# Kernel tuning notes

Measured on AMD Instinct MI355X. Metric: run time of the kernel, lower is better.

Reference implementation:

```python
import jax, jax.numpy as jnp
import numpy as np

B, L, D_IN, H, N, NL = 16, 5000, 12, 256, 32, 4  # N = d_state//2 complex modes


def layer_norm(x, g, b, eps=1e-5):
    m = x.mean(-1, keepdims=True)
    v = ((x - m) ** 2).mean(-1, keepdims=True)
    return (x - m) * jax.lax.rsqrt(v + eps) * g + b


def s4d_kernel(log_dt, logA_re, A_im, Cp, length):
    # S4D-style diagonal SSM kernel (ZOH discretization), conjugate-symmetric -> 2*real
    dt = jnp.exp(log_dt)                      # (H,)
    A = -jnp.exp(logA_re) + 1j * A_im         # (H, N)
    C = Cp[..., 0] + 1j * Cp[..., 1]          # (H, N)
    dtA = A * dt[:, None]                     # (H, N)
    Ct = C * (jnp.exp(dtA) - 1.0) / A         # (H, N)
    V = jnp.exp(dtA[:, :, None] * jnp.arange(length, dtype=log_dt.dtype))  # (H, N, L) Vandermonde
    return 2.0 * jnp.einsum('hn,hnl->hl', Ct, V).real  # (H, L)


def s4_block(u, log_dt, logA_re, A_im, Cp, D, W_glu, b_glu):
    # u: (B, L, H), transposed=False convention
    length = u.shape[1]
    K = s4d_kernel(log_dt, logA_re, A_im, Cp, length)     # (H, L)
    n_fft = 2 * length
    k_f = jnp.fft.rfft(K, n=n_fft)                        # (H, F)
    u_f = jnp.fft.rfft(u, n=n_fft, axis=1)                # (B, F, H)
    y = jnp.fft.irfft(u_f * k_f.T[None], n=n_fft, axis=1)[:, :length]  # causal conv
    y = y + u * D                                         # skip connection
    y = jax.nn.gelu(y)
    y = y @ W_glu + b_glu                                 # (B, L, 2H)
    return jax.nn.glu(y, axis=-1)                         # (B, L, H)


def setup_inputs() -> dict:
    key = jax.random.key(0)
    ks = jax.random.split(key, 8)
    dt_min, dt_max = 1e-3, 1e-1
    log_dt = np.log(dt_min) + jax.random.uniform(ks[2], (NL, H)) * (np.log(dt_max) - np.log(dt_min))
    A_im = jnp.broadcast_to(np.pi * jnp.arange(N, dtype=jnp.float32), (NL, H, N)).copy()
    return {
        'x': jax.random.normal(ks[0], (B, L, D_IN), jnp.float32),
        'W_in': jax.random.normal(ks[1], (D_IN, H), jnp.float32) / np.sqrt(D_IN),
        'b_in': jnp.zeros((H,), jnp.float32),
        'ln_g': jnp.ones((NL, H), jnp.float32),
        'ln_b': jnp.zeros((NL, H), jnp.float32),
        'log_dt': log_dt.astype(jnp.float32),
        'logA_re': jnp.full((NL, H, N), np.log(0.5), jnp.float32),
        'A_im': A_im,
        'Cp': jax.random.normal(ks[3], (NL, H, N, 2), jnp.float32) * (0.5 ** 0.5),
        'D': jax.random.normal(ks[4], (NL, H), jnp.float32),
        'W_glu': jax.random.normal(ks[5], (NL, H, 2 * H), jnp.float32) / np.sqrt(H),
        'b_glu': jnp.zeros((NL, 2 * H), jnp.float32),
        'fn_g': jnp.ones((H,), jnp.float32),
        'fn_b': jnp.zeros((H,), jnp.float32),
    }


def reference(x, W_in, b_in, ln_g, ln_b, log_dt, logA_re, A_im, Cp, D, W_glu, b_glu, fn_g, fn_b):
    x = x @ W_in + b_in  # (B, L, H)
    for i in range(NL):
        z = layer_norm(x, ln_g[i], ln_b[i])  # prenorm
        residual = z
        y = s4_block(z, log_dt[i], logA_re[i], A_im[i], Cp[i], D[i], W_glu[i], b_glu[i])
        x = y + residual  # dropout is identity in eval
    return layer_norm(x, fn_g, fn_b)
```

## Files before the change

### kernel.cpp

```cpp
#include <hip/hip_runtime.h>
#include <math.h>

#define BB 16
#define LL 5000
#define DIN 12
#define HH 256
#define NN 32
#define NLAYER 4
#define LC 128
#define NCH 40
#define TAIL 8
#define COLS (BB*NCH)
#define NROWS (BB*LL)
#define KU 192

typedef __attribute__((ext_vector_type(8))) _Float16 f16x8;
typedef __attribute__((ext_vector_type(4))) float f32x4;

__device__ __forceinline__ float fast_gelu(float a) {
  float z = fmaf(0.0713548163f * a, a * a, 1.5957691216f * a);
  float e = __expf(-z);
  return a * __builtin_amdgcn_rcpf(1.0f + e);
}

__device__ __forceinline__ unsigned pk2h(float a, float b) {
  union { _Float16 h[2]; unsigned u; } x;
  x.h[0] = (_Float16)a; x.h[1] = (_Float16)b;
  return x.u;
}

__device__ __forceinline__ float2 upk2(unsigned u) {
  union { unsigned u; _Float16 h[2]; } x;
  x.u = u;
  return make_float2((float)x.h[0], (float)x.h[1]);
}

__global__ __launch_bounds__(128) void paramT_kernel(
    const float* __restrict__ log_dt, const float* __restrict__ logA_re,
    const float* __restrict__ A_im, const float* __restrict__ Cp,
    const float* __restrict__ Dv, int l,
    _Float16* __restrict__ Tc, _Float16* __restrict__ V, float* __restrict__ WLc) {
  int h = blockIdx.x;
  int t = threadIdx.x;
  __shared__ float s_are[NN], s_aim[NN], s_cre[NN], s_cim[NN];
  __shared__ float s_K[128];
  if (t < NN) {
    int n = t;
    int idx = (l * HH + h) * NN + n;
    float dt = expf(log_dt[l * HH + h]);
    float Are = -expf(logA_re[idx]);
    float Aim = A_im[idx];
    float are = Are * dt, aim = Aim * dt;
    float e = expf(are);
    float wre = e * cosf(aim), wim = e * sinf(aim);
    float cr = Cp[2 * idx], ci = Cp[2 * idx + 1];
    float nre = wre - 1.0f, nim = wim;
    float tre = cr * nre - ci * nim;
    float tim = cr * nim + ci * nre;
    float inv = 1.0f / (Are * Are + Aim * Aim);
    s_are[n] = are; s_aim[n] = aim;
    s_cre[n] = 2.0f * (tre * Are + tim * Aim) * inv;
    s_cim[n] = 2.0f * (tim * Are - tre * Aim) * inv;
    float eL = expf(128.0f * are);
    float ang = 128.0f * aim;
    WLc[h * 64 + 2 * n] = eL * cosf(ang);
    WLc[h * 64 + 2 * n + 1] = eL * sinf(ang);
  }
  __syncthreads();
  {
    float ksum = 0.0f;
    unsigned* brow = (unsigned*)(Tc + ((size_t)h * 128 + t) * KU + 128);
    for (int n = 0; n < NN; n++) {
      float are = s_are[n], aim = s_aim[n];
      float cre = s_cre[n], cim = s_cim[n];
      float ft = (float)t;
      float E = expf(are * ft);
      float a = aim * ft;
      float wtre = E * cosf(a), wtim = E * sinf(a);
      ksum = fmaf(cre, wtre, ksum);
      ksum = fmaf(-cim, wtim, ksum);
      float ew = expf(are);
      float wre = ew * cosf(aim), wim = ew * sinf(aim);
      float wpre = wtre * wre - wtim * wim;
      float wpim = wtre * wim + wtim * wre;
      float bre = cre * wpre - cim * wpim;
      float bim = -(cre * wpim + cim * wpre);
      brow[n] = pk2h(bre, bim);
      float fk = (float)(127 - t);
      float E2 = expf(are * fk);
      float a2 = aim * fk;
      V[((size_t)h * 64 + 2 * n) * 128 + t] = (_Float16)(E2 * cosf(a2));
      V[((size_t)h * 64 + 2 * n + 1) * 128 + t] = (_Float16)(E2 * sinf(a2));
    }
    s_K[t] = ksum;
  }
  __syncthreads();
  float D = Dv[l * HH + h];
  unsigned* row = (unsigned*)(Tc + ((size_t)h * 128 + t) * KU);
  for (int q = 0; q < 64; q++) {
    float v0 = 0.0f, v1 = 0.0f;
    int d0 = t - 2 * q;
    int d1 = d0 - 1;
    if (d0 >= 0) v0 = s_K[d0] + (d0 == 0 ? D : 0.0f);
    if (d1 >= 0) v1 = s_K[d1] + (d1 == 0 ? D : 0.0f);
    row[q] = pk2h(v0, v1);
  }
}

__global__ __launch_bounds__(256) void wt_kernel(
    const float* __restrict__ W, _Float16* __restrict__ Wt) {
  int gid = blockIdx.x * 256 + threadIdx.x;
  int l = gid >> 9, col = gid & 511;
  const float* w = W + (size_t)l * HH * 512 + col;
  _Float16* o = Wt + (size_t)gid * HH;
  for (int k = 0; k < HH; k++) o[k] = (_Float16)(w[(size_t)k * 512]);
}

__global__ __launch_bounds__(256) void proj_kernel(
    const float* __restrict__ x, const float* __restrict__ Win,
    const float* __restrict__ bin, _Float16* __restrict__ X) {
  int tp = threadIdx.x & 127, rs = threadIdx.x >> 7;
  int h0 = 2 * tp;
  float w0[DIN], w1[DIN];
#pragma unroll
  for (int k = 0; k < DIN; k++) {
    w0[k] = Win[k * HH + h0];
    w1[k] = Win[k * HH + h0 + 1];
  }
  float b0 = bin[h0], b1 = bin[h0 + 1];
  for (int row = blockIdx.x * 2 + rs; row < NROWS; row += gridDim.x * 2) {
    float a0 = b0, a1 = b1;
#pragma unroll
    for (int k = 0; k < DIN; k++) {
      float xv = x[(size_t)row * DIN + k];
      a0 = fmaf(xv, w0[k], a0);
      a1 = fmaf(xv, w1[k], a1);
    }
    *(unsigned*)(X + (size_t)row * HH + h0) = pk2h(a0, a1);
  }
}

__global__ __launch_bounds__(256) void ln_kernel(
    const _Float16* __restrict__ in, float* __restrict__ out,
    const float* __restrict__ g, const float* __restrict__ b) {
  int wave = threadIdx.x >> 6, lane = threadIdx.x & 63;
  int row = blockIdx.x * 4 + wave;
  uint2 pv = *(const uint2*)(in + (size_t)row * HH + 4 * lane);
  float2 v01 = upk2(pv.x), v23 = upk2(pv.y);
  float s = v01.x + v01.y + v23.x + v23.y;
  float q = v01.x * v01.x + v01.y * v01.y + v23.x * v23.x + v23.y * v23.y;
#pragma unroll
  for (int m = 1; m < 64; m <<= 1) { s += __shfl_xor(s, m); q += __shfl_xor(q, m); }
  float mean = s * (1.0f / HH);
  float var = q * (1.0f / HH) - mean * mean;
  float rstd = rsqrtf(var + 1e-5f);
  float4 gg = ((const float4*)g)[lane];
  float4 bb = ((const float4*)b)[lane];
  float4 o;
  o.x = (v01.x - mean) * rstd * gg.x + bb.x;
  o.y = (v01.y - mean) * rstd * gg.y + bb.y;
  o.z = (v23.x - mean) * rstd * gg.z + bb.z;
  o.w = (v23.y - mean) * rstd * gg.w + bb.w;
  ((float4*)(out + (size_t)row * HH))[lane] = o;
}

__global__ __launch_bounds__(256) void lnU_kernel(
    _Float16* __restrict__ stream, _Float16* __restrict__ U,
    const float* __restrict__ g, const float* __restrict__ b) {
  __shared__ unsigned short Ut[64][260];
  int col = blockIdx.x;
  int bI = col / NCH, cI = col % NCH;
  int len = (cI == NCH - 1) ? TAIL : 128;
  int wave = threadIdx.x >> 6, lane = threadIdx.x & 63;
  float4 gg = ((const float4*)g)[lane];
  float4 bv = ((const float4*)b)[lane];
  size_t base = ((size_t)bI * LL + (size_t)cI * 128) * HH;
#pragma unroll
  for (int half = 0; half < 2; half++) {
    if (half) __syncthreads();
    int t0 = half * 64;
    int lenh = len - t0;
    lenh = lenh < 0 ? 0 : (lenh > 64 ? 64 : lenh);
    for (int idx = threadIdx.x; idx < (64 - lenh) * 260; idx += 256) {
      int r = idx / 260;
      Ut[lenh + r][idx - r * 260] = 0;
    }
    for (int it = 0; it < 16; it++) {
      int tl = it * 4 + wave;
      if (tl < lenh) {
        int tau = t0 + tl;
        uint2 pv = *(const uint2*)(stream + base + (size_t)tau * HH + 4 * lane);
        float2 v01 = upk2(pv.x), v23 = upk2(pv.y);
        float s = v01.x + v01.y + v23.x + v23.y;
        float q = v01.x * v01.x + v01.y * v01.y + v23.x * v23.x + v23.y * v23.y;
#pragma unroll
        for (int m = 1; m < 64; m <<= 1) { s += __shfl_xor(s, m); q += __shfl_xor(q, m); }
        float mean = s * (1.0f / HH);
        float var = q * (1.0f / HH) - mean * mean;
        float rstd = rsqrtf(var + 1e-5f);
        float o0 = (v01.x - mean) * rstd * gg.x + bv.x;
        float o1 = (v01.y - mean) * rstd * gg.y + bv.y;
        float o2 = (v23.x - mean) * rstd * gg.z + bv.z;
        float o3 = (v23.y - mean) * rstd * gg.w + bv.w;
        uint2 p;
        p.x = pk2h(o0, o1);
        p.y = pk2h(o2, o3);
        *(uint2*)(stream + base + (size_t)tau * HH + 4 * lane) = p;
        *(uint2*)&Ut[tl][4 * lane] = p;
      }
    }
    __syncthreads();
    for (int rep = 0; rep < 8; rep++) {
      int linear = rep * 256 + threadIdx.x;
      int h = linear >> 3, ub = linear & 7;
      unsigned* dst = (unsigned*)(U + ((size_t)h * COLS + col) * KU) + half * 32;
#pragma unroll
      for (int s2 = 0; s2 < 4; s2++) {
        int u = ub + s2 * 8;
        dst[u] = (unsigned)Ut[2 * u][h] | ((unsigned)Ut[2 * u + 1][h] << 16);
      }
    }
  }
}

__global__ __launch_bounds__(256) void gemmAC_kernel(
    const _Float16* __restrict__ V, _Float16* __restrict__ U,
    const float* __restrict__ WLc) {
  __shared__ float smf[4096];
  _Float16* As = (_Float16*)smf;
  _Float16* Bs = As + 64 * 72;
  float* Ps = smf;
  int h = blockIdx.x, b = blockIdx.y;
  int t = threadIdx.x;
  int w = t >> 6, lane = t & 63, lr = lane & 15, quad = lane >> 4;
  f32x4 acc[3];
#pragma unroll
  for (int j = 0; j < 3; j++) acc[j] = (f32x4)(0.0f);

  for (int kt = 0; kt < 128; kt += 64) {
#pragma unroll
    for (int i = 0; i < 2; i++) {
      int idx = t + 256 * i;
      int m = idx >> 3, q = idx & 7;
      *(uint4*)&As[m * 72 + q * 8] =
          *(const uint4*)(V + ((size_t)h * 64 + m) * 128 + kt + q * 8);
    }
#pragma unroll
    for (int i = 0; i < 2; i++) {
      int idx = t + 256 * i;
      if (idx < 384) {
        int jj = idx >> 3, q = idx & 7;
        uint4 v = make_uint4(0u, 0u, 0u, 0u);
        if (jj < NCH)
          v = *(const uint4*)(U + ((size_t)h * COLS + (size_t)b * NCH + jj) * KU + kt + q * 8);
        *(uint4*)&Bs[jj * 72 + q * 8] = v;
      }
    }
    __syncthreads();
#pragma unroll
    for (int ks = 0; ks < 2; ks++) {
      f16x8 af = *(const f16x8*)&As[(w * 16 + lr) * 72 + ks * 32 + quad * 8];
#pragma unroll
      for (int j = 0; j < 3; j++) {
        f16x8 bf = *(const f16x8*)&Bs[(j * 16 + lr) * 72 + ks * 32 + quad * 8];
        acc[j] = __builtin_amdgcn_mfma_f32_16x16x32_f16(af, bf, acc[j], 0, 0, 0);
      }
    }
    __syncthreads();
  }
#pragma unroll
  for (int j = 0; j < 3; j++)
#pragma unroll
    for (int r = 0; r < 4; r++)
      Ps[(w * 16 + quad * 4 + r) * 49 + j * 16 + lr] = acc[j][r];
  __syncthreads();

  if (t < 32) {
    int n = t;
    float wre = WLc[h * 64 + 2 * n], wim = WLc[h * 64 + 2 * n + 1];
    float cre = 0.0f, cim = 0.0f;
    _Float16* u = U + ((size_t)h * COLS + (size_t)b * NCH) * KU + 128 + 2 * n;
    for (int c = 0; c < NCH; c++) {
      float vre = Ps[(2 * n) * 49 + c];
      float vim = Ps[(2 * n + 1) * 49 + c];
      *(unsigned*)(u + (size_t)c * KU) = pk2h(cre, cim);
      float nre = fmaf(wre, cre, vre) - wim * cim;
      float nim = fmaf(wre, cim, vim) + wim * cre;
      cre = nre; cim = nim;
    }
  }
}

__global__ __launch_bounds__(256) void gemmC_kernel(
    const _Float16* __restrict__ Tc, const _Float16* __restrict__ U,
    _Float16* __restrict__ Yt) {
  __shared__ _Float16 As[128 * 72];
  __shared__ _Float16 Bs[128 * 72];
  int h = blockIdx.x, c0 = blockIdx.y * 128;
  int t = threadIdx.x;
  int w = t >> 6, lane = t & 63, lr = lane & 15, quad = lane >> 4;
  f32x4 acc[2][8];
#pragma unroll
  for (int i = 0; i < 2; i++)
#pragma unroll
    for (int j = 0; j < 8; j++) acc[i][j] = (f32x4)(0.0f);

  for (int kt = 0; kt < KU; kt += 64) {
#pragma unroll
    for (int i = 0; i < 4; i++) {
      int idx = t + 256 * i;
      int m = idx >> 3, q = idx & 7;
      *(uint4*)&As[m * 72 + q * 8] =
          *(const uint4*)(Tc + ((size_t)h * 128 + m) * KU + kt + q * 8);
    }
#pragma unroll
    for (int i = 0; i < 4; i++) {
      int idx = t + 256 * i;
      int jj = idx >> 3, q = idx & 7;
      *(uint4*)&Bs[jj * 72 + q * 8] =
          *(const uint4*)(U + ((size_t)h * COLS + c0 + jj) * KU + kt + q * 8);
    }
    __syncthreads();
#pragma unroll
    for (int ks = 0; ks < 2; ks++) {
      f16x8 af[2], bf[8];
#pragma unroll
      for (int i = 0; i < 2; i++)
        af[i] = *(const f16x8*)&As[(w * 32 + i * 16 + lr) * 72 + ks * 32 + quad * 8];
#pragma unroll
      for (int j = 0; j < 8; j++)
        bf[j] = *(const f16x8*)&Bs[(j * 16 + lr) * 72 + ks * 32 + quad * 8];
#pragma unroll
      for (int i = 0; i < 2; i++)
#pragma unroll
        for (int j = 0; j < 8; j++)
          acc[i][j] = __builtin_amdgcn_mfma_f32_16x16x32_f16(af[i], bf[j], acc[i][j], 0, 0, 0);
    }
    __syncthreads();
  }
#pragma unroll
  for (int i = 0; i < 2; i++) {
#pragma unroll
    for (int j = 0; j < 8; j++) {
      int tb = w * 32 + i * 16 + quad * 4;
      int colx = c0 + j * 16 + lr;
      f32x4 a = acc[i][j];
      uint2 r;
      r.x = pk2h(fast_gelu(a[0]), fast_gelu(a[1]));
      r.y = pk2h(fast_gelu(a[2]), fast_gelu(a[3]));
      *(uint2*)(Yt + ((size_t)h * COLS + colx) * 128 + tb) = r;
    }
  }
}

__global__ __launch_bounds__(256) void gemm_glu_mfma(
    const _Float16* __restrict__ Yt, const _Float16* __restrict__ Wt,
    const float* __restrict__ bg, _Float16* __restrict__ Xio) {
  __shared__ uint4 smemq[2304];
  _Float16* As = (_Float16*)smemq;
  _Float16* Bs = (_Float16*)smemq + 128 * 64;
  float* gl = (float*)smemq;
  int t = threadIdx.x;
  int col = blockIdx.x;
  int bI = col / NCH, pt = col % NCH;
  int len = (pt == NCH - 1) ? TAIL : 128;
  size_t row0 = (size_t)bI * LL + (size_t)pt * 128;
  int c0 = blockIdx.y * 64;
  int w = t >> 6, lane = t & 63;
  int lr = lane & 15, quad = lane >> 4;
  int rh = w & 1, ch = w >> 1;
  int oct = lane & 15, hq = lane >> 4;
  int godd = hq & 1;
  int jbase = godd * 4;
  int goct = (oct + (oct >> 3)) & 7;
  f32x4 acc[4][4];
#pragma unroll
  for (int i = 0; i < 4; i++)
#pragma unroll
    for (int j = 0; j < 4; j++) acc[i][j] = (f32x4)(0.0f);

  int jb[4] = {ch * 32, ch * 32 + 16, 64 + ch * 32, 80 + ch * 32};

  for (int kt = 0; kt < HH; kt += 64) {
#pragma unroll
    for (int p = 0; p < 4; p++) {
      int hl = p * 16 + w * 4 + hq;
      uint4 v = *(const uint4*)(Yt + ((size_t)(kt + hl) * COLS + col) * 128 + oct * 8);
      uint4 pv;
      pv.x = __shfl_xor((int)v.x, 16);
      pv.y = __shfl_xor((int)v.y, 16);
      pv.z = __shfl_xor((int)v.z, 16);
      pv.w = __shfl_xor((int)v.w, 16);
      unsigned a0 = godd ? pv.z : v.x;
      unsigned a1 = godd ? pv.w : v.y;
      unsigned b0 = godd ? v.z : pv.x;
      unsigned b1 = godd ? v.w : pv.y;
      unsigned p0 = (a0 & 0xffffu) | (b0 << 16);
      unsigned p1 = (a0 >> 16) | (b0 & 0xffff0000u);
      unsigned p2 = (a1 & 0xffffu) | (b1 << 16);
      unsigned p3 = (a1 >> 16) | (b1 & 0xffff0000u);
      int soc = (hl >> 3) ^ goct;
      char* basep = (char*)As + oct * 1024 + (hl & 6) * 2;
      { int j = jbase;     *(unsigned*)(basep + j * 128 + ((soc ^ j) * 16)) = p0; }
      { int j = jbase + 1; *(unsigned*)(basep + j * 128 + ((soc ^ j) * 16)) = p1; }
      { int j = jbase + 2; *(unsigned*)(basep + j * 128 + ((soc ^ j) * 16)) = p2; }
      { int j = jbase + 3; *(unsigned*)(basep + j * 128 + ((soc ^ j) * 16)) = p3; }
    }
#pragma unroll
    for (int i = 0; i < 4; i++) {
      int idx = t + 256 * i;
      int jj = idx >> 3, q = idx & 7;
      int colw = (jj < 64) ? (c0 + jj) : (192 + c0 + jj);
      *(uint4*)&Bs[jj * 72 + q * 8] =
          *(const uint4*)(Wt + (size_t)colw * HH + kt + q * 8);
    }
    __syncthreads();
#pragma unroll
    for (int ks = 0; ks < 2; ks++) {
      f16x8 af[4], bf[4];
#pragma unroll
      for (int i = 0; i < 4; i++) {
        int tt = rh * 64 + i * 16 + lr;
        int ttg = tt >> 3;
        int so = (ks * 4 + quad) ^ (tt & 7) ^ ((ttg + (ttg >> 3)) & 7);
        af[i] = *(const f16x8*)((const char*)As + tt * 128 + so * 16);
      }
#pragma unroll
      for (int j = 0; j < 4; j++)
        bf[j] = *(const f16x8*)&Bs[(jb[j] + lr) * 72 + ks * 32 + quad * 8];
#pragma unroll
      for (int i = 0; i < 4; i++)
#pragma unroll
        for (int j = 0; j < 4; j++)
          acc[i][j] = __builtin_amdgcn_mfma_f32_16x16x32_f16(af[i], bf[j], acc[i][j], 0, 0, 0);
    }
    __syncthreads();
  }

#pragma unroll
  for (int i = 0; i < 4; i++) {
#pragma unroll
    for (int r = 0; r < 4; r++) {
      int rowl = rh * 64 + i * 16 + quad * 4 + r;
#pragma unroll
      for (int jp = 0; jp < 2; jp++) {
        int hl = ch * 32 + jp * 16 + lr;
        int h = c0 + hl;
        float g1 = acc[i][jp][r] + bg[h];
        float g2 = acc[i][jp + 2][r] + bg[256 + h];
        float sig = __builtin_amdgcn_rcpf(1.0f + __expf(-g2));
        gl[rowl * 68 + hl] = g1 * sig;
      }
    }
  }
  __syncthreads();

#pragma unroll
  for (int rep = 0; rep < 4; rep++) {
    int lin = rep * 256 + t;
    int rowl = lin >> 3, hc = lin & 7;
    if (rowl < len) {
      size_t row = row0 + rowl;
      int hb = c0 + hc * 8;
      uint4 zv = *(const uint4*)(Xio + row * HH + hb);
      float2 z01 = upk2(zv.x), z23 = upk2(zv.y), z45 = upk2(zv.z), z67 = upk2(zv.w);
      const float* gp = &gl[rowl * 68 + hc * 8];
      uint4 r;
      r.x = pk2h(gp[0] + z01.x, gp[1] + z01.y);
      r.y = pk2h(gp[2] + z23.x, gp[3] + z23.y);
      r.z = pk2h(gp[4] + z45.x, gp[5] + z45.y);
      r.w = pk2h(gp[6] + z67.x, gp[7] + z67.y);
      *(uint4*)(Xio + row * HH + hb) = r;
    }
  }
}

extern "C" void kernel_launch(void* const* d_in, const int* in_sizes, int n_in,
                              void* d_out, int out_size, void* d_ws, size_t ws_size,
                              hipStream_t stream) {
  const float* x      = (const float*)d_in[0];
  const float* Win    = (const float*)d_in[1];
  const float* bin    = (const float*)d_in[2];
  const float* ln_g   = (const float*)d_in[3];
  const float* ln_b   = (const float*)d_in[4];
  const float* log_dt = (const float*)d_in[5];
  const float* logA   = (const float*)d_in[6];
  const float* A_im   = (const float*)d_in[7];
  const float* Cp     = (const float*)d_in[8];
  const float* Dv     = (const float*)d_in[9];
  const float* Wglu   = (const float*)d_in[10];
  const float* bglu   = (const float*)d_in[11];
  const float* fn_g   = (const float*)d_in[12];
  const float* fn_b   = (const float*)d_in[13];
  float* out = (float*)d_out;
  float* ws = (float*)d_ws;

  _Float16* Xs = (_Float16*)ws;
  float* Pf = ws + (size_t)NROWS * HH;
  _Float16* Tc = (_Float16*)(Pf + (size_t)HH * COLS * 64);
  _Float16* V  = Tc + (size_t)HH * 128 * KU;
  _Float16* U  = V + (size_t)HH * 64 * 128;
  _Float16* Wt = U + (size_t)HH * COLS * KU;
  float* WLc = (float*)(Wt + (size_t)NLAYER * 512 * HH);
  _Float16* Yt  = (_Float16*)Pf;

  wt_kernel<<<(NLAYER * 512) / 256, 256, 0, stream>>>(Wglu, Wt);
  proj_kernel<<<2048, 256, 0, stream>>>(x, Win, bin, Xs);

  for (int l = 0; l < NLAYER; l++) {
    paramT_kernel<<<HH, 128, 0, stream>>>(log_dt, logA, A_im, Cp, Dv, l, Tc, V, WLc);
    lnU_kernel<<<COLS, 256, 0, stream>>>(Xs, U, ln_g + l * HH, ln_b + l * HH);
    gemmAC_kernel<<<dim3(HH, BB), 256, 0, stream>>>(V, U, WLc);
    gemmC_kernel<<<dim3(HH, COLS / 128), 256, 0, stream>>>(Tc, U, Yt);
    gemm_glu_mfma<<<dim3(COLS, 4), 256, 0, stream>>>(
        Yt, Wt + (size_t)l * 512 * HH, bglu + (size_t)l * 2 * HH, Xs);
  }
  ln_kernel<<<NROWS / 4, 256, 0, stream>>>(Xs, out, fn_g, fn_b);
}
```

Measured before the change: 875.5 us.

## Fuse chunk-state scan and intra-chunk GEMM into one kernel per head-batch

Merges gemmAC and gemmC into a single kernel per (head, batch) block. The U chunk tile is kept in shared memory, and the scanned carry states are written there directly instead of round-tripping through global U. This removes one kernel launch per layer and the global write/read of the carry states and U. In exchange, the C GEMM now runs with a smaller N tile of 48 columns (40 used, so some MFMA work is padding), each block reloads the Tc weights, and shared memory use rises, which may lower occupancy.

```diff
diff --git a/kernel.cpp b/kernel.cpp
--- a/kernel.cpp
+++ b/kernel.cpp
@@ -223,38 +223,38 @@
   }
 }
 
-__global__ __launch_bounds__(256) void gemmAC_kernel(
-    const _Float16* __restrict__ V, _Float16* __restrict__ U,
-    const float* __restrict__ WLc) {
-  __shared__ float smf[4096];
-  _Float16* As = (_Float16*)smf;
-  _Float16* Bs = As + 64 * 72;
-  float* Ps = smf;
+__global__ __launch_bounds__(256) void gemmACC_kernel(
+    const _Float16* __restrict__ V, const _Float16* __restrict__ Tc,
+    const _Float16* __restrict__ U, const float* __restrict__ WLc,
+    _Float16* __restrict__ Yt) {
+  __shared__ uint4 smemq[2352];
+  _Float16* As = (_Float16*)smemq;
+  _Float16* Bs = As + 128 * 72;
+  float* Ps = (float*)As;
   int h = blockIdx.x, b = blockIdx.y;
   int t = threadIdx.x;
   int w = t >> 6, lane = t & 63, lr = lane & 15, quad = lane >> 4;
-  f32x4 acc[3];
-#pragma unroll
-  for (int j = 0; j < 3; j++) acc[j] = (f32x4)(0.0f);
-
-  for (int kt = 0; kt < 128; kt += 64) {
+
+#pragma unroll
+  for (int i = 0; i < 3; i++) {
+    int idx = t + 256 * i;
+    int jj = idx >> 4, q = idx & 15;
+    uint4 v = make_uint4(0u, 0u, 0u, 0u);
+    if (jj < NCH)
+      v = *(const uint4*)(U + ((size_t)h * COLS + (size_t)b * NCH + jj) * KU + q * 8);
+    *(uint4*)&Bs[jj * 200 + q * 8] = v;
+  }
+
+  f32x4 accA[3];
+#pragma unroll
+  for (int j = 0; j < 3; j++) accA[j] = (f32x4)(0.0f);
+  for (int kt = 0; kt < 2; kt++) {
 #pragma unroll
     for (int i = 0; i < 2; i++) {
       int idx = t + 256 * i;
       int m = idx >> 3, q = idx & 7;
       *(uint4*)&As[m * 72 + q * 8] =
-          *(const uint4*)(V + ((size_t)h * 64 + m) * 128 + kt + q * 8);
-    }
-#pragma unroll
-    for (int i = 0; i < 2; i++) {
-      int idx = t + 256 * i;
-      if (idx < 384) {
-        int jj = idx >> 3, q = idx & 7;
-        uint4 v = make_uint4(0u, 0u, 0u, 0u);
-        if (jj < NCH)
-          v = *(const uint4*)(U + ((size_t)h * COLS + (size_t)b * NCH + jj) * KU + kt + q * 8);
-        *(uint4*)&Bs[jj * 72 + q * 8] = v;
-      }
+          *(const uint4*)(V + ((size_t)h * 64 + m) * 128 + kt * 64 + q * 8);
     }
     __syncthreads();
 #pragma unroll
@@ -262,8 +262,8 @@
       f16x8 af = *(const f16x8*)&As[(w * 16 + lr) * 72 + ks * 32 + quad * 8];
 #pragma unroll
       for (int j = 0; j < 3; j++) {
-        f16x8 bf = *(const f16x8*)&Bs[(j * 16 + lr) * 72 + ks * 32 + quad * 8];
-        acc[j] = __builtin_amdgcn_mfma_f32_16x16x32_f16(af, bf, acc[j], 0, 0, 0);
+        f16x8 bf = *(const f16x8*)&Bs[(j * 16 + lr) * 200 + kt * 64 + ks * 32 + quad * 8];
+        accA[j] = __builtin_amdgcn_mfma_f32_16x16x32_f16(af, bf, accA[j], 0, 0, 0);
       }
     }
     __syncthreads();
@@ -272,83 +272,71 @@
   for (int j = 0; j < 3; j++)
 #pragma unroll
     for (int r = 0; r < 4; r++)
-      Ps[(w * 16 + quad * 4 + r) * 49 + j * 16 + lr] = acc[j][r];
+      Ps[(w * 16 + quad * 4 + r) * 49 + j * 16 + lr] = accA[j][r];
   __syncthreads();
 
   if (t < 32) {
     int n = t;
     float wre = WLc[h * 64 + 2 * n], wim = WLc[h * 64 + 2 * n + 1];
     float cre = 0.0f, cim = 0.0f;
-    _Float16* u = U + ((size_t)h * COLS + (size_t)b * NCH) * KU + 128 + 2 * n;
     for (int c = 0; c < NCH; c++) {
       float vre = Ps[(2 * n) * 49 + c];
       float vim = Ps[(2 * n + 1) * 49 + c];
-      *(unsigned*)(u + (size_t)c * KU) = pk2h(cre, cim);
+      *(unsigned*)&Bs[c * 200 + 128 + 2 * n] = pk2h(cre, cim);
       float nre = fmaf(wre, cre, vre) - wim * cim;
       float nim = fmaf(wre, cim, vim) + wim * cre;
       cre = nre; cim = nim;
     }
-  }
-}
-
-__global__ __launch_bounds__(256) void gemmC_kernel(
-    const _Float16* __restrict__ Tc, const _Float16* __restrict__ U,
-    _Float16* __restrict__ Yt) {
-  __shared__ _Float16 As[128 * 72];
-  __shared__ _Float16 Bs[128 * 72];
-  int h = blockIdx.x, c0 = blockIdx.y * 128;
-  int t = threadIdx.x;
-  int w = t >> 6, lane = t & 63, lr = lane & 15, quad = lane >> 4;
-  f32x4 acc[2][8];
+#pragma unroll
+    for (int c = NCH; c < 48; c++)
+      *(unsigned*)&Bs[c * 200 + 128 + 2 * n] = 0u;
+  }
+  __syncthreads();
+
+  f32x4 accC[2][3];
 #pragma unroll
   for (int i = 0; i < 2; i++)
 #pragma unroll
-    for (int j = 0; j < 8; j++) acc[i][j] = (f32x4)(0.0f);
-
-  for (int kt = 0; kt < KU; kt += 64) {
+    for (int j = 0; j < 3; j++) accC[i][j] = (f32x4)(0.0f);
+  for (int kt = 0; kt < 3; kt++) {
 #pragma unroll
     for (int i = 0; i < 4; i++) {
       int idx = t + 256 * i;
       int m = idx >> 3, q = idx & 7;
       *(uint4*)&As[m * 72 + q * 8] =
-          *(const uint4*)(Tc + ((size_t)h * 128 + m) * KU + kt + q * 8);
-    }
-#pragma unroll
-    for (int i = 0; i < 4; i++) {
-      int idx = t + 256 * i;
-      int jj = idx >> 3, q = idx & 7;
-      *(uint4*)&Bs[jj * 72 + q * 8] =
-          *(const uint4*)(U + ((size_t)h * COLS + c0 + jj) * KU + kt + q * 8);
+          *(const uint4*)(Tc + ((size_t)h * 128 + m) * KU + kt * 64 + q * 8);
     }
     __syncthreads();
 #pragma unroll
     for (int ks = 0; ks < 2; ks++) {
-      f16x8 af[2], bf[8];
+      f16x8 af[2], bf[3];
 #pragma unroll
       for (int i = 0; i < 2; i++)
         af[i] = *(const f16x8*)&As[(w * 32 + i * 16 + lr) * 72 + ks * 32 + quad * 8];
 #pragma unroll
-      for (int j = 0; j < 8; j++)
-        bf[j] = *(const f16x8*)&Bs[(j * 16 + lr) * 72 + ks * 32 + quad * 8];
+      for (int j = 0; j < 3; j++)
+        bf[j] = *(const f16x8*)&Bs[(j * 16 + lr) * 200 + kt * 64 + ks * 32 + quad * 8];
 #pragma unroll
       for (int i = 0; i < 2; i++)
 #pragma unroll
-        for (int j = 0; j < 8; j++)
-          acc[i][j] = __builtin_amdgcn_mfma_f32_16x16x32_f16(af[i], bf[j], acc[i][j], 0, 0, 0);
+        for (int j = 0; j < 3; j++)
+          accC[i][j] = __builtin_amdgcn_mfma_f32_16x16x32_f16(af[i], bf[j], accC[i][j], 0, 0, 0);
     }
     __syncthreads();
   }
 #pragma unroll
   for (int i = 0; i < 2; i++) {
 #pragma unroll
-    for (int j = 0; j < 8; j++) {
+    for (int j = 0; j < 3; j++) {
       int tb = w * 32 + i * 16 + quad * 4;
-      int colx = c0 + j * 16 + lr;
-      f32x4 a = acc[i][j];
-      uint2 r;
-      r.x = pk2h(fast_gelu(a[0]), fast_gelu(a[1]));
-      r.y = pk2h(fast_gelu(a[2]), fast_gelu(a[3]));
-      *(uint2*)(Yt + ((size_t)h * COLS + colx) * 128 + tb) = r;
+      int cl = j * 16 + lr;
+      if (cl < NCH) {
+        f32x4 a = accC[i][j];
+        uint2 r;
+        r.x = pk2h(fast_gelu(a[0]), fast_gelu(a[1]));
+        r.y = pk2h(fast_gelu(a[2]), fast_gelu(a[3]));
+        *(uint2*)(Yt + ((size_t)h * COLS + (size_t)b * NCH + cl) * 128 + tb) = r;
+      }
     }
   }
 }
@@ -510,8 +498,7 @@
   for (int l = 0; l < NLAYER; l++) {
     paramT_kernel<<<HH, 128, 0, stream>>>(log_dt, logA, A_im, Cp, Dv, l, Tc, V, WLc);
     lnU_kernel<<<COLS, 256, 0, stream>>>(Xs, U, ln_g + l * HH, ln_b + l * HH);
-    gemmAC_kernel<<<dim3(HH, BB), 256, 0, stream>>>(V, U, WLc);
-    gemmC_kernel<<<dim3(HH, COLS / 128), 256, 0, stream>>>(Tc, U, Yt);
+    gemmACC_kernel<<<dim3(HH, BB), 256, 0, stream>>>(V, Tc, U, WLc, Yt);
     gemm_glu_mfma<<<dim3(COLS, 4), 256, 0, stream>>>(
         Yt, Wt + (size_t)l * 512 * HH, bglu + (size_t)l * 2 * HH, Xs);
   }
```

New measurement: 845.7 us. 1.04x faster.
